# Kernel tuning notes

Hardware: AMD Instinct MI355X
Metric: run time of the kernel (lower is better)

The kernel has to match this reference:

```python
import jax, jax.numpy as jnp
import numpy as np

B = 16384
F = 50
NUM_USERS = 100000
NUM_ITEMS = 100000
NUM_UFEAT = 2000
NUM_IFEAT = 2000
D = 128


def setup_inputs() -> dict:
    key = jax.random.key(0)
    ks = jax.random.split(key, 10)
    return {
        "user_ids": jax.random.randint(ks[0], (B,), 0, NUM_USERS, dtype=jnp.int32),
        "item_ids": jax.random.randint(ks[1], (B,), 0, NUM_ITEMS, dtype=jnp.int32),
        "user_feature_indices": jax.random.randint(ks[2], (B, F), 0, NUM_UFEAT, dtype=jnp.int32),
        "user_feature_values": jax.random.uniform(ks[3], (B, F), dtype=jnp.float32),
        "item_feature_indices": jax.random.randint(ks[4], (B, F), 0, NUM_IFEAT, dtype=jnp.int32),
        "item_feature_values": jax.random.uniform(ks[5], (B, F), dtype=jnp.float32),
        "user_emb": jax.random.normal(ks[6], (NUM_USERS, D), dtype=jnp.float32) * 0.01,
        "item_emb": jax.random.normal(ks[7], (NUM_ITEMS, D), dtype=jnp.float32) * 0.01,
        "user_feat_emb": jax.random.normal(ks[8], (NUM_UFEAT, D), dtype=jnp.float32) * 0.01,
        "item_feat_emb": jax.random.normal(ks[9], (NUM_IFEAT, D), dtype=jnp.float32) * 0.01,
    }


def reference(user_ids, item_ids, user_feature_indices, user_feature_values,
              item_feature_indices, item_feature_values,
              user_emb, item_emb, user_feat_emb, item_feat_emb):
    # Base id embeddings: [B, D]
    u = user_emb[user_ids]
    v = item_emb[item_ids]
    # Weighted ragged feature sums (padded dense form): [B, F, D] x [B, F] -> [B, D]
    u = u + jnp.einsum("bfd,bf->bd", user_feat_emb[user_feature_indices], user_feature_values)
    v = v + jnp.einsum("bfd,bf->bd", item_feat_emb[item_feature_indices], item_feature_values)
    # Dot-product prediction: [B]
    return jnp.sum(u * v, axis=1)
```

## Files before the change

kernel.cpp:

```cpp
#include <hip/hip_runtime.h>
#include <hip/hip_fp16.h>

#define BATCH  16384
#define NFEAT  50
#define DIM    128
#define NROWS  2000
#define TBL_HALFS (NROWS * DIM)
#define WS_NEEDED (2u * TBL_HALFS * 2u)

__global__ __launch_bounds__(256) void k1_convert(
    const float* __restrict__ ufe,
    const float* __restrict__ ife,
    ushort*      __restrict__ wsa)
{
    const int u = blockIdx.x * 256 + threadIdx.x;
    const int t   = (u >= 32000) ? 1 : 0;
    const int rem = u - t * 32000;
    const int r = rem >> 4, c = rem & 15;
    const float* src = (t ? ife : ufe) + (size_t)r * DIM + c * 4;
    const float4 a = *reinterpret_cast<const float4*>(src);
    const float4 b = *reinterpret_cast<const float4*>(src + 64);
    __half2 hh[4];
    hh[0] = __floats2half2_rn(a.x, a.y);
    hh[1] = __floats2half2_rn(a.z, a.w);
    hh[2] = __floats2half2_rn(b.x, b.y);
    hh[3] = __floats2half2_rn(b.z, b.w);
    *reinterpret_cast<uint4*>(wsa + ((size_t)(t * NROWS + r) * 16 + c) * 8) =
        *reinterpret_cast<uint4*>(hh);
}

__global__ __launch_bounds__(256) void mf_dot_q(
    const int*    __restrict__ user_ids,
    const int*    __restrict__ item_ids,
    const int*    __restrict__ ufi,
    const float*  __restrict__ ufv,
    const int*    __restrict__ ifi,
    const float*  __restrict__ ifv,
    const float*  __restrict__ user_emb,
    const float*  __restrict__ item_emb,
    const ushort* __restrict__ wsa,
    float*        __restrict__ out)
{
    __shared__ uint meta[2 * 16 * NFEAT];

    const int tid = threadIdx.x;
    const int eb  = blockIdx.x * 16;

    #pragma unroll
    for (int rme = 0; rme < 4; ++rme) {
        const int k = rme * 256 + tid;
        if (k < 16 * NFEAT) {
            const uint  iu = (uint)ufi[(size_t)eb * NFEAT + k];
            const float vu = ufv[(size_t)eb * NFEAT + k];
            meta[k] = (iu & 0xffffu) |
                      ((uint)__half_as_ushort(__float2half_rn(vu)) << 16);
            const uint  ii = (uint)ifi[(size_t)eb * NFEAT + k];
            const float vi = ifv[(size_t)eb * NFEAT + k];
            meta[16 * NFEAT + k] = (ii & 0xffffu) |
                      ((uint)__half_as_ushort(__float2half_rn(vi)) << 16);
        }
    }
    __syncthreads();

    const int lane = tid & 63;
    const int w    = tid >> 6;
    const int q    = lane & 15;
    const int el   = w * 4 + (lane >> 4);
    const int e    = eb + el;

    const int uid = user_ids[e];
    const int iid = item_ids[e];
    const float4 ua = *reinterpret_cast<const float4*>(user_emb + (size_t)uid * DIM + q * 4);
    const float4 ub = *reinterpret_cast<const float4*>(user_emb + (size_t)uid * DIM + 64 + q * 4);
    const float4 va = *reinterpret_cast<const float4*>(item_emb + (size_t)iid * DIM + q * 4);
    const float4 vb = *reinterpret_cast<const float4*>(item_emb + (size_t)iid * DIM + 64 + q * 4);

    const uint* __restrict__ mu = meta + el * NFEAT;
    const uint* __restrict__ mi = meta + 16 * NFEAT + el * NFEAT;
    const ushort* __restrict__ tu_base = wsa;
    const ushort* __restrict__ ti_base = wsa + TBL_HALFS;

    __half2 au0 = __float2half2_rn(0.f), au1 = au0, au2 = au0, au3 = au0;
    __half2 ai0 = au0, ai1 = au0, ai2 = au0, ai3 = au0;

    #pragma unroll 10
    for (int f = 0; f < NFEAT; ++f) {
        const uint wu = mu[f];
        const uint wi = mi[f];

        const uint4 tu = *reinterpret_cast<const uint4*>(
            tu_base + (size_t)(wu & 0xffffu) * DIM + q * 8);
        const uint4 ti = *reinterpret_cast<const uint4*>(
            ti_base + (size_t)(wi & 0xffffu) * DIM + q * 8);

        const __half2 vu2 = __half2half2(__ushort_as_half((ushort)(wu >> 16)));
        const __half2 vi2 = __half2half2(__ushort_as_half((ushort)(wi >> 16)));

        const __half2* th = reinterpret_cast<const __half2*>(&tu);
        au0 = __hfma2(th[0], vu2, au0);
        au1 = __hfma2(th[1], vu2, au1);
        au2 = __hfma2(th[2], vu2, au2);
        au3 = __hfma2(th[3], vu2, au3);
        const __half2* ih = reinterpret_cast<const __half2*>(&ti);
        ai0 = __hfma2(ih[0], vi2, ai0);
        ai1 = __hfma2(ih[1], vi2, ai1);
        ai2 = __hfma2(ih[2], vi2, ai2);
        ai3 = __hfma2(ih[3], vi2, ai3);
    }

    const float2 du0 = __half22float2(au0), du1 = __half22float2(au1);
    const float2 du2 = __half22float2(au2), du3 = __half22float2(au3);
    const float2 dv0 = __half22float2(ai0), dv1 = __half22float2(ai1);
    const float2 dv2 = __half22float2(ai2), dv3 = __half22float2(ai3);

    float dot = (ua.x + du0.x) * (va.x + dv0.x)
              + (ua.y + du0.y) * (va.y + dv0.y)
              + (ua.z + du1.x) * (va.z + dv1.x)
              + (ua.w + du1.y) * (va.w + dv1.y)
              + (ub.x + du2.x) * (vb.x + dv2.x)
              + (ub.y + du2.y) * (vb.y + dv2.y)
              + (ub.z + du3.x) * (vb.z + dv3.x)
              + (ub.w + du3.y) * (vb.w + dv3.y);

    #pragma unroll
    for (int off = 8; off > 0; off >>= 1)
        dot += __shfl_xor(dot, off);

    if (q == 0) out[e] = dot;
}

__global__ __launch_bounds__(256) void mf_dot_fallback(
    const int*   __restrict__ user_ids,
    const int*   __restrict__ item_ids,
    const int*   __restrict__ ufi,
    const float* __restrict__ ufv,
    const int*   __restrict__ ifi,
    const float* __restrict__ ifv,
    const float* __restrict__ user_emb,
    const float* __restrict__ item_emb,
    const float* __restrict__ user_feat_emb,
    const float* __restrict__ item_feat_emb,
    float*       __restrict__ out)
{
    const int tid  = threadIdx.x;
    const int lane = tid & 63;
    const int half = lane >> 5;
    const int sl   = lane & 31;
    const int d0   = sl * 4;

    int wv = (int)((blockIdx.x * blockDim.x + tid) >> 6);
    wv = __builtin_amdgcn_readfirstlane(wv);
    const int b0 = wv * 2, b1 = b0 + 1;
    const int b  = half ? b1 : b0;

    const int uid0 = user_ids[b0], uid1 = user_ids[b1];
    const int iid0 = item_ids[b0], iid1 = item_ids[b1];
    const int urow = half ? uid1 : uid0;
    const int irow = half ? iid1 : iid0;

    float4 uacc = *reinterpret_cast<const float4*>(user_emb + (size_t)urow * DIM + d0);
    float4 vacc = *reinterpret_cast<const float4*>(item_emb + (size_t)irow * DIM + d0);

    #pragma unroll 10
    for (int f = 0; f < NFEAT; ++f) {
        const int   ui0 = ufi[b0 * NFEAT + f], ui1 = ufi[b1 * NFEAT + f];
        const float uv0 = ufv[b0 * NFEAT + f], uv1 = ufv[b1 * NFEAT + f];
        const int   ii0 = ifi[b0 * NFEAT + f], ii1 = ifi[b1 * NFEAT + f];
        const float iv0 = ifv[b0 * NFEAT + f], iv1 = ifv[b1 * NFEAT + f];

        const int   ur = half ? ui1 : ui0;
        const float uw = half ? uv1 : uv0;
        const int   ir = half ? ii1 : ii0;
        const float iw = half ? iv1 : iv0;

        const float4 ue = *reinterpret_cast<const float4*>(user_feat_emb + (size_t)ur * DIM + d0);
        const float4 ie = *reinterpret_cast<const float4*>(item_feat_emb + (size_t)ir * DIM + d0);

        uacc.x = fmaf(uw, ue.x, uacc.x);
        uacc.y = fmaf(uw, ue.y, uacc.y);
        uacc.z = fmaf(uw, ue.z, uacc.z);
        uacc.w = fmaf(uw, ue.w, uacc.w);
        vacc.x = fmaf(iw, ie.x, vacc.x);
        vacc.y = fmaf(iw, ie.y, vacc.y);
        vacc.z = fmaf(iw, ie.z, vacc.z);
        vacc.w = fmaf(iw, ie.w, vacc.w);
    }

    float dot = uacc.x * vacc.x + uacc.y * vacc.y + uacc.z * vacc.z + uacc.w * vacc.w;
    #pragma unroll
    for (int off = 16; off > 0; off >>= 1)
        dot += __shfl_xor(dot, off);
    if (sl == 0) out[b] = dot;
}

extern "C" void kernel_launch(void* const* d_in, const int* in_sizes, int n_in,
                              void* d_out, int out_size, void* d_ws, size_t ws_size,
                              hipStream_t stream) {
    const int*   user_ids      = (const int*)  d_in[0];
    const int*   item_ids      = (const int*)  d_in[1];
    const int*   ufi           = (const int*)  d_in[2];
    const float* ufv           = (const float*)d_in[3];
    const int*   ifi           = (const int*)  d_in[4];
    const float* ifv           = (const float*)d_in[5];
    const float* user_emb      = (const float*)d_in[6];
    const float* item_emb      = (const float*)d_in[7];
    const float* user_feat_emb = (const float*)d_in[8];
    const float* item_feat_emb = (const float*)d_in[9];
    float* out = (float*)d_out;

    if (ws_size >= WS_NEEDED) {
        ushort* wsa = (ushort*)d_ws;
        k1_convert<<<250, 256, 0, stream>>>(user_feat_emb, item_feat_emb, wsa);
        mf_dot_q<<<BATCH / 16, 256, 0, stream>>>(
            user_ids, item_ids, ufi, ufv, ifi, ifv,
            user_emb, item_emb, wsa, out);
    } else {
        mf_dot_fallback<<<BATCH / 8, 256, 0, stream>>>(
            user_ids, item_ids, ufi, ufv, ifi, ifv,
            user_emb, item_emb, user_feat_emb, item_feat_emb, out);
    }
}
```

Baseline: 27.95 us.

## Fuse table conversion and dot kernel into one cooperative grid-sync kernel

Merges the fp32-to-fp16 feature-table conversion and the main gather/dot kernel into one persistent cooperative kernel. The grid is sized from occupancy, the conversion runs grid-stride, a grid-wide sync follows, and then the 16-row tiles are processed grid-stride. This removes one kernel launch and the gap between the two kernels. In exchange it adds a grid barrier, occupancy queries on the host for every call, and a grid capped at the resident block count. The old two-kernel path stays as a fallback if the cooperative launch fails.

```diff
diff --git a/kernel.cpp b/kernel.cpp
--- a/kernel.cpp
+++ b/kernel.cpp
@@ -1,5 +1,8 @@
 #include <hip/hip_runtime.h>
 #include <hip/hip_fp16.h>
+#include <hip/hip_cooperative_groups.h>
+
+namespace cg = cooperative_groups;
 
 #define BATCH  16384
 #define NFEAT  50
@@ -7,15 +10,14 @@
 #define NROWS  2000
 #define TBL_HALFS (NROWS * DIM)
 #define WS_NEEDED (2u * TBL_HALFS * 2u)
-
-__global__ __launch_bounds__(256) void k1_convert(
-    const float* __restrict__ ufe,
-    const float* __restrict__ ife,
-    ushort*      __restrict__ wsa)
-{
-    const int u = blockIdx.x * 256 + threadIdx.x;
-    const int t   = (u >= 32000) ? 1 : 0;
-    const int rem = u - t * 32000;
+#define NCHUNKS (2 * NROWS * 16)
+
+__device__ __forceinline__ void convert_chunk(
+    int u, const float* __restrict__ ufe, const float* __restrict__ ife,
+    ushort* __restrict__ wsa)
+{
+    const int t   = (u >= NCHUNKS / 2) ? 1 : 0;
+    const int rem = u - t * (NCHUNKS / 2);
     const int r = rem >> 4, c = rem & 15;
     const float* src = (t ? ife : ufe) + (size_t)r * DIM + c * 4;
     const float4 a = *reinterpret_cast<const float4*>(src);
@@ -29,22 +31,15 @@
         *reinterpret_cast<uint4*>(hh);
 }
 
-__global__ __launch_bounds__(256) void mf_dot_q(
-    const int*    __restrict__ user_ids,
-    const int*    __restrict__ item_ids,
-    const int*    __restrict__ ufi,
-    const float*  __restrict__ ufv,
-    const int*    __restrict__ ifi,
-    const float*  __restrict__ ifv,
-    const float*  __restrict__ user_emb,
-    const float*  __restrict__ item_emb,
-    const ushort* __restrict__ wsa,
-    float*        __restrict__ out)
-{
-    __shared__ uint meta[2 * 16 * NFEAT];
-
+__device__ __forceinline__ void tile_body(
+    int eb, uint* meta,
+    const int* __restrict__ user_ids, const int* __restrict__ item_ids,
+    const int* __restrict__ ufi, const float* __restrict__ ufv,
+    const int* __restrict__ ifi, const float* __restrict__ ifv,
+    const float* __restrict__ user_emb, const float* __restrict__ item_emb,
+    const ushort* __restrict__ wsa, float* __restrict__ out)
+{
     const int tid = threadIdx.x;
-    const int eb  = blockIdx.x * 16;
 
     #pragma unroll
     for (int rme = 0; rme < 4; ++rme) {
@@ -87,15 +82,12 @@
     for (int f = 0; f < NFEAT; ++f) {
         const uint wu = mu[f];
         const uint wi = mi[f];
-
         const uint4 tu = *reinterpret_cast<const uint4*>(
             tu_base + (size_t)(wu & 0xffffu) * DIM + q * 8);
         const uint4 ti = *reinterpret_cast<const uint4*>(
             ti_base + (size_t)(wi & 0xffffu) * DIM + q * 8);
-
         const __half2 vu2 = __half2half2(__ushort_as_half((ushort)(wu >> 16)));
         const __half2 vi2 = __half2half2(__ushort_as_half((ushort)(wi >> 16)));
-
         const __half2* th = reinterpret_cast<const __half2*>(&tu);
         au0 = __hfma2(th[0], vu2, au0);
         au1 = __hfma2(th[1], vu2, au1);
@@ -127,6 +119,63 @@
         dot += __shfl_xor(dot, off);
 
     if (q == 0) out[e] = dot;
+}
+
+__global__ __launch_bounds__(256) void mf_fused_gs(
+    const float*  __restrict__ ufe,
+    const float*  __restrict__ ife,
+    const int*    __restrict__ user_ids,
+    const int*    __restrict__ item_ids,
+    const int*    __restrict__ ufi,
+    const float*  __restrict__ ufv,
+    const int*    __restrict__ ifi,
+    const float*  __restrict__ ifv,
+    const float*  __restrict__ user_emb,
+    const float*  __restrict__ item_emb,
+    ushort*       __restrict__ wsa,
+    float*        __restrict__ out)
+{
+    __shared__ uint meta[2 * 16 * NFEAT];
+    const int tid    = threadIdx.x;
+    const int stride = gridDim.x * 256;
+
+    for (int u = blockIdx.x * 256 + tid; u < NCHUNKS; u += stride)
+        convert_chunk(u, ufe, ife, wsa);
+
+    __threadfence();
+    cg::this_grid().sync();
+
+    for (int eb = blockIdx.x * 16; eb < BATCH; eb += gridDim.x * 16) {
+        tile_body(eb, meta, user_ids, item_ids, ufi, ufv, ifi, ifv,
+                  user_emb, item_emb, wsa, out);
+        __syncthreads();
+    }
+}
+
+__global__ __launch_bounds__(256) void k1_convert(
+    const float* __restrict__ ufe,
+    const float* __restrict__ ife,
+    ushort*      __restrict__ wsa)
+{
+    const int u = blockIdx.x * 256 + threadIdx.x;
+    if (u < NCHUNKS) convert_chunk(u, ufe, ife, wsa);
+}
+
+__global__ __launch_bounds__(256) void mf_dot_q(
+    const int*    __restrict__ user_ids,
+    const int*    __restrict__ item_ids,
+    const int*    __restrict__ ufi,
+    const float*  __restrict__ ufv,
+    const int*    __restrict__ ifi,
+    const float*  __restrict__ ifv,
+    const float*  __restrict__ user_emb,
+    const float*  __restrict__ item_emb,
+    const ushort* __restrict__ wsa,
+    float*        __restrict__ out)
+{
+    __shared__ uint meta[2 * 16 * NFEAT];
+    tile_body(blockIdx.x * 16, meta, user_ids, item_ids, ufi, ufv, ifi, ifv,
+              user_emb, item_emb, wsa, out);
 }
 
 __global__ __launch_bounds__(256) void mf_dot_fallback(
@@ -196,27 +245,59 @@
 extern "C" void kernel_launch(void* const* d_in, const int* in_sizes, int n_in,
                               void* d_out, int out_size, void* d_ws, size_t ws_size,
                               hipStream_t stream) {
-    const int*   user_ids      = (const int*)  d_in[0];
-    const int*   item_ids      = (const int*)  d_in[1];
-    const int*   ufi           = (const int*)  d_in[2];
-    const float* ufv           = (const float*)d_in[3];
-    const int*   ifi           = (const int*)  d_in[4];
-    const float* ifv           = (const float*)d_in[5];
-    const float* user_emb      = (const float*)d_in[6];
-    const float* item_emb      = (const float*)d_in[7];
-    const float* user_feat_emb = (const float*)d_in[8];
-    const float* item_feat_emb = (const float*)d_in[9];
+    const float* ufe = (const float*)d_in[8];
+    const float* ife = (const float*)d_in[9];
+    const int* user_ids = (const int*)d_in[0];
+    const int* item_ids = (const int*)d_in[1];
+    const int* ufi = (const int*)d_in[2];
+    const float* ufv = (const float*)d_in[3];
+    const int* ifi = (const int*)d_in[4];
+    const float* ifv = (const float*)d_in[5];
+    const float* user_emb = (const float*)d_in[6];
+    const float* item_emb = (const float*)d_in[7];
     float* out = (float*)d_out;
 
-    if (ws_size >= WS_NEEDED) {
-        ushort* wsa = (ushort*)d_ws;
-        k1_convert<<<250, 256, 0, stream>>>(user_feat_emb, item_feat_emb, wsa);
+    if (ws_size < WS_NEEDED) {
+        mf_dot_fallback<<<BATCH / 8, 256, 0, stream>>>(
+            user_ids, item_ids, ufi, ufv, ifi, ifv,
+            user_emb, item_emb, ufe, ife, out);
+        return;
+    }
+
+    ushort* wsa = (ushort*)d_ws;
+
+    int grid = 0;
+    {
+        int occ = 0, ncu = 0, dev = 0;
+        (void)hipGetDevice(&dev);
+        (void)hipOccupancyMaxActiveBlocksPerMultiprocessor(
+            &occ, (const void*)mf_fused_gs, 256, 0);
+        (void)hipDeviceGetAttribute(&ncu, hipDeviceAttributeMultiprocessorCount, dev);
+        if (occ > 0 && ncu > 0) {
+            long cap = (long)occ * (long)ncu;
+            grid = (int)(cap < (BATCH / 16) ? cap : (BATCH / 16));
+        }
+    }
+
+    bool launched = false;
+    if (grid > 0) {
+        void* args[] = {
+            (void*)&ufe, (void*)&ife,
+            (void*)&user_ids, (void*)&item_ids,
+            (void*)&ufi, (void*)&ufv, (void*)&ifi, (void*)&ifv,
+            (void*)&user_emb, (void*)&item_emb,
+            (void*)&wsa, (void*)&out,
+        };
+        hipError_t err = hipLaunchCooperativeKernel(
+            (const void*)mf_fused_gs, dim3(grid), dim3(256), args, 0, stream);
+        launched = (err == hipSuccess);
+        if (!launched) (void)hipGetLastError();
+    }
+
+    if (!launched) {
+        k1_convert<<<(NCHUNKS + 255) / 256, 256, 0, stream>>>(ufe, ife, wsa);
         mf_dot_q<<<BATCH / 16, 256, 0, stream>>>(
             user_ids, item_ids, ufi, ufv, ifi, ifv,
             user_emb, item_emb, wsa, out);
-    } else {
-        mf_dot_fallback<<<BATCH / 8, 256, 0, stream>>>(
-            user_ids, item_ids, ufi, ufv, ifi, ifv,
-            user_emb, item_emb, user_feat_emb, item_feat_emb, out);
-    }
-}
+    }
+}
```

Result: slower. 111.5 us (+298.8%).
